# Optimization experiments

Measured on AMD Instinct MI355X. Metric: run time of the kernel, lower is better.

The kernel has to match this reference:

```python
import jax, jax.numpy as jnp
import numpy as np

N_NODES = 50000
N_EDGES = 800000
D_IN = 64
D_OUT = 64


def setup_inputs() -> dict:
    key = jax.random.key(0)
    ks = jax.random.split(key, 7)
    features = jax.random.normal(ks[0], (N_NODES, D_IN), dtype=jnp.float32)
    # Linear(in,out,bias=False) weight: (out_features, in_features)
    W = jax.random.normal(ks[1], (D_OUT, D_IN), dtype=jnp.float32) / np.sqrt(D_IN)
    bias = jnp.zeros((D_OUT,), dtype=jnp.float32)
    skip_weight = jnp.ones((D_OUT,), dtype=jnp.float32)
    # sparse normalized adjacency as an edge list with scalar weights
    edge_src = jax.random.randint(ks[2], (N_EDGES,), 0, N_NODES, dtype=jnp.int32)
    edge_dst = jax.random.randint(ks[3], (N_EDGES,), 0, N_NODES, dtype=jnp.int32)
    edge_weight = jax.random.uniform(ks[4], (N_EDGES,), dtype=jnp.float32)
    return {
        "features": features,
        "W": W,
        "bias": bias,
        "skip_weight": skip_weight,
        "edge_weight": edge_weight,
        "edge_src": edge_src,
        "edge_dst": edge_dst,
    }


def reference(features, W, bias, skip_weight, edge_weight, edge_src, edge_dst):
    # Feature transform: x @ W^T  -> (n, out_features)
    h = jnp.einsum("nd,od->no", features, W)
    # Skip term: elementwise scale of transformed features
    skip = h * skip_weight
    # Sparse SpMM: aggregate weighted neighbor messages
    msgs = h[edge_src] * edge_weight[:, None]          # (E, out)
    agg = jax.ops.segment_sum(msgs, edge_dst, num_segments=N_NODES)  # (n, out)
    out = skip + agg + bias
    return jax.nn.selu(out)
```

## Files before the change

kernel.cpp:

```cpp
#include <hip/hip_runtime.h>
#include <math.h>

#define N_NODES 50000
#define N_EDGES 800000
#define D 64
#define NB2 782
#define BCAP2 2048
#define EPB 4096
#define NSCAT 196
#define CAPB 32
#define SLAB (NSCAT * CAPB)
#define GROWS 128
#define NGEMM ((N_NODES + GROWS - 1) / GROWS)

__device__ __forceinline__ float selu_f(float x) {
    const float scale = 1.0507009873554805f;
    const float alpha = 1.6732632423543772f;
    return x > 0.0f ? scale * x : scale * alpha * expm1f(x);
}

__device__ __forceinline__ unsigned int f2bf(float x) {
    unsigned int u = __float_as_uint(x);
    u += 0x7FFFu + ((u >> 16) & 1u);
    return u >> 16;
}

__device__ __forceinline__ float bf2f(unsigned int b) {
    return __uint_as_float(b << 16);
}

__global__ __launch_bounds__(1024) void fused_gemm_scatter(const float* __restrict__ feat,
                                                           const float* __restrict__ W,
                                                           const int* __restrict__ edst,
                                                           const int* __restrict__ esrc,
                                                           const float* __restrict__ ew,
                                                           unsigned short* __restrict__ hb,
                                                           int* __restrict__ cnts,
                                                           int2* __restrict__ pay) {
    extern __shared__ char smem[];
    const int tid = threadIdx.x;

    if (blockIdx.x < NSCAT) {
        int* hist    = (int*)smem;
        int* lexcl   = hist + NB2;
        int* waveAgg = lexcl + NB2;
        int2* stage  = (int2*)(waveAgg + 16);

        const int wid = tid >> 6;
        const int lane = tid & 63;
        const int e0 = blockIdx.x * EPB;
        const int cntb = min(EPB, N_EDGES - e0);

        for (int i = tid; i < NB2; i += 1024) hist[i] = 0;
        __syncthreads();

        int2 rec[4];
        int rb[4];
#pragma unroll
        for (int k = 0; k < 4; ++k) {
            const int idx = k * 1024 + tid;
            rb[k] = -1;
            if (idx < cntb) {
                const int e = e0 + idx;
                const int dst = edst[e];
                const int b = dst >> 6;
                rb[k] = b;
                rec[k] = make_int2((esrc[e] & 0xFFFF) | ((dst & 63) << 16) | (b << 22),
                                   __float_as_int(ew[e]));
                atomicAdd(&hist[b], 1);
            }
        }
        __syncthreads();

        const int v = (tid < NB2) ? hist[tid] : 0;
        int incl = v;
#pragma unroll
        for (int off = 1; off < 64; off <<= 1) {
            const int t = __shfl_up(incl, off);
            if (lane >= off) incl += t;
        }
        if (lane == 63) waveAgg[wid] = incl;
        __syncthreads();
        if (wid == 0) {
            const int wv = (lane < 16) ? waveAgg[lane] : 0;
            int wincl = wv;
#pragma unroll
            for (int off = 1; off < 16; off <<= 1) {
                const int t = __shfl_up(wincl, off);
                if (lane >= off) wincl += t;
            }
            if (lane < 16) waveAgg[lane] = wincl - wv;
        }
        __syncthreads();
        if (tid < NB2) {
            const int excl = incl - v + waveAgg[wid];
            lexcl[tid] = excl;
            hist[tid] = excl;
            cnts[blockIdx.x * NB2 + tid] = v;
        }
        __syncthreads();

#pragma unroll
        for (int k = 0; k < 4; ++k) {
            if (rb[k] >= 0) {
                const int p = atomicAdd(&hist[rb[k]], 1);
                stage[p] = rec[k];
            }
        }
        __syncthreads();

        for (int i = tid; i < cntb; i += 1024) {
            const int2 r = stage[i];
            const int b = ((unsigned int)r.x) >> 22;
            const int off = i - lexcl[b];
            if (off < CAPB) pay[(size_t)b * SLAB + blockIdx.x * CAPB + off] = r;
        }
    } else {
        float* Wt = (float*)smem;
        float* Sf = Wt + 64 * 68;
        const int base = (blockIdx.x - NSCAT) * GROWS;

        for (int i = tid; i < D * D; i += 1024) {
            int o = i >> 6, d = i & 63;
            Wt[d * 68 + o] = W[i];
        }
        for (int i = tid; i < GROWS * D; i += 1024) {
            int r = i >> 6, c = i & 63;
            int row = base + r;
            Sf[r * 68 + c] = (row < N_NODES) ? feat[(size_t)row * D + c] : 0.0f;
        }
        __syncthreads();

        const int r = tid >> 3;
        const int cg = tid & 7;
        const int row = base + r;
        if (row >= N_NODES) return;

        float4 a0 = {0, 0, 0, 0}, a1 = {0, 0, 0, 0};
        const float* WtC = Wt + cg * 8;
        const float* SfR = Sf + r * 68;
#pragma unroll 8
        for (int k = 0; k < D; ++k) {
            const float f = SfR[k];
            const float4 w0 = *(const float4*)(WtC + k * 68);
            const float4 w1 = *(const float4*)(WtC + k * 68 + 4);
            a0.x += f * w0.x; a0.y += f * w0.y; a0.z += f * w0.z; a0.w += f * w0.w;
            a1.x += f * w1.x; a1.y += f * w1.y; a1.z += f * w1.z; a1.w += f * w1.w;
        }

        uint4 p;
        p.x = f2bf(a0.x) | (f2bf(a0.y) << 16);
        p.y = f2bf(a0.z) | (f2bf(a0.w) << 16);
        p.z = f2bf(a1.x) | (f2bf(a1.y) << 16);
        p.w = f2bf(a1.z) | (f2bf(a1.w) << 16);
        *(uint4*)(hb + (size_t)row * D + cg * 8) = p;
    }
}

__global__ __launch_bounds__(1024) void sort_agg(const int* __restrict__ cnts,
                                                 const int2* __restrict__ pay,
                                                 const unsigned short* __restrict__ hb,
                                                 const float* __restrict__ bias,
                                                 const float* __restrict__ skipw,
                                                 float* __restrict__ out) {
    __shared__ int2 stage[BCAP2];
    __shared__ int2 sorted[BCAP2];
    __shared__ int cntS[NSCAT];
    __shared__ int runoff[NSCAT];
    __shared__ int waveAgg[16];
    __shared__ int cntB[64], begB[64], curB[64];

    const int b = blockIdx.x;
    const int tid = threadIdx.x;
    const int wid = tid >> 6;
    const int lane = tid & 63;
    const int2* payb = pay + (size_t)b * SLAB;

    if (tid < 64) cntB[tid] = 0;

    const int c = (tid < NSCAT) ? cnts[tid * NB2 + b] : 0;

    int incl = c;
#pragma unroll
    for (int off = 1; off < 64; off <<= 1) {
        const int t = __shfl_up(incl, off);
        if (lane >= off) incl += t;
    }
    if (lane == 63) waveAgg[wid] = incl;
    __syncthreads();
    if (wid == 0) {
        const int wv = (lane < 16) ? waveAgg[lane] : 0;
        int wincl = wv;
#pragma unroll
        for (int off = 1; off < 16; off <<= 1) {
            const int t = __shfl_up(wincl, off);
            if (lane >= off) wincl += t;
        }
        if (lane < 16) waveAgg[lane] = wincl - wv;
    }
    __syncthreads();
    if (tid < NSCAT) {
        cntS[tid] = c;
        runoff[tid] = incl - c + waveAgg[wid];
    }
    __syncthreads();

    for (int i = tid; i < NSCAT * CAPB; i += 1024) {
        const int blk = i >> 5;
        const int pos = i & (CAPB - 1);
        if (pos < cntS[blk]) {
            const int p = runoff[blk] + pos;
            if (p < BCAP2) {
                const int2 r = payb[i];
                stage[p] = r;
                atomicAdd(&cntB[(r.x >> 16) & 63], 1);
            }
        }
    }
    __syncthreads();

    const int total = min(runoff[NSCAT - 1] + cntS[NSCAT - 1], BCAP2);

    if (tid < 64) {
        const int v = cntB[tid];
        int inc2 = v;
#pragma unroll
        for (int off = 1; off < 64; off <<= 1) {
            const int t = __shfl_up(inc2, off);
            if (tid >= off) inc2 += t;
        }
        const int excl = inc2 - v;
        begB[tid] = excl;
        curB[tid] = excl;
    }
    __syncthreads();

    for (int i = tid; i < total; i += 1024) {
        const int2 r = stage[i];
        const int p = atomicAdd(&curB[(r.x >> 16) & 63], 1);
        sorted[p] = r;
    }
    __syncthreads();

    const int half = lane >> 5;
    const int sl = lane & 31;
    const float2 kv = ((const float2*)skipw)[sl];
    const float2 bv = ((const float2*)bias)[sl];

    for (int nn = 0; nn < 4; ++nn) {
        const int nl = wid * 4 + nn;
        const int node = (b << 6) + nl;
        if (node >= N_NODES) break;

        const int beg = begB[nl];
        const int deg = cntB[nl];

        float a0x = 0.f, a0y = 0.f, a1x = 0.f, a1y = 0.f;
        float a2x = 0.f, a2y = 0.f, a3x = 0.f, a3y = 0.f;

        int j = 0;
        for (; j + 7 < deg; j += 8) {
            const int2 r0 = sorted[beg + j + 0 + half];
            const int2 r1 = sorted[beg + j + 2 + half];
            const int2 r2 = sorted[beg + j + 4 + half];
            const int2 r3 = sorted[beg + j + 6 + half];
            const unsigned int g0 = *(const unsigned int*)(hb + ((size_t)(r0.x & 0xFFFF) << 6) + sl * 2);
            const unsigned int g1 = *(const unsigned int*)(hb + ((size_t)(r1.x & 0xFFFF) << 6) + sl * 2);
            const unsigned int g2 = *(const unsigned int*)(hb + ((size_t)(r2.x & 0xFFFF) << 6) + sl * 2);
            const unsigned int g3 = *(const unsigned int*)(hb + ((size_t)(r3.x & 0xFFFF) << 6) + sl * 2);
            const float w0 = __int_as_float(r0.y);
            const float w1 = __int_as_float(r1.y);
            const float w2 = __int_as_float(r2.y);
            const float w3 = __int_as_float(r3.y);
            a0x += bf2f(g0 & 0xFFFF) * w0;  a0y += bf2f(g0 >> 16) * w0;
            a1x += bf2f(g1 & 0xFFFF) * w1;  a1y += bf2f(g1 >> 16) * w1;
            a2x += bf2f(g2 & 0xFFFF) * w2;  a2y += bf2f(g2 >> 16) * w2;
            a3x += bf2f(g3 & 0xFFFF) * w3;  a3y += bf2f(g3 >> 16) * w3;
        }
        for (; j + 1 < deg; j += 2) {
            const int2 r = sorted[beg + j + half];
            const unsigned int g = *(const unsigned int*)(hb + ((size_t)(r.x & 0xFFFF) << 6) + sl * 2);
            const float w = __int_as_float(r.y);
            a0x += bf2f(g & 0xFFFF) * w;  a0y += bf2f(g >> 16) * w;
        }
        if (j < deg) {
            const int2 r = sorted[beg + j];
            const unsigned int g = *(const unsigned int*)(hb + ((size_t)(r.x & 0xFFFF) << 6) + sl * 2);
            const float w = __int_as_float(r.y);
            const float m = (half == 0) ? 1.0f : 0.0f;
            a1x += bf2f(g & 0xFFFF) * w * m;  a1y += bf2f(g >> 16) * w * m;
        }

        float sx = (a0x + a1x) + (a2x + a3x);
        float sy = (a0y + a1y) + (a2y + a3y);
        sx += __shfl_xor(sx, 32);
        sy += __shfl_xor(sy, 32);

        if (half == 0) {
            const unsigned int hn = *(const unsigned int*)(hb + ((size_t)node << 6) + sl * 2);
            float2 o;
            o.x = selu_f(bf2f(hn & 0xFFFF) * kv.x + bv.x + sx);
            o.y = selu_f(bf2f(hn >> 16) * kv.y + bv.y + sy);
            ((float2*)(out + ((size_t)node << 6)))[sl] = o;
        }
    }
}

extern "C" void kernel_launch(void* const* d_in, const int* in_sizes, int n_in,
                              void* d_out, int out_size, void* d_ws, size_t ws_size,
                              hipStream_t stream) {
    const float* feat  = (const float*)d_in[0];
    const float* W     = (const float*)d_in[1];
    const float* bias  = (const float*)d_in[2];
    const float* skipw = (const float*)d_in[3];
    const float* ew    = (const float*)d_in[4];
    const int*   esrc  = (const int*)d_in[5];
    const int*   edst  = (const int*)d_in[6];
    float* out = (float*)d_out;

    int2*           pay  = (int2*)d_ws;
    unsigned short* hb   = (unsigned short*)(pay + (size_t)NB2 * SLAB);
    int*            cnts = (int*)(hb + (size_t)N_NODES * D);

    const size_t smem = (size_t)(64 * 68 + GROWS * 68) * sizeof(float);
    fused_gemm_scatter<<<NSCAT + NGEMM, 1024, smem, stream>>>(feat, W, edst, esrc, ew,
                                                              hb, cnts, pay);

    sort_agg<<<NB2, 1024, 0, stream>>>(cnts, pay, hb, bias, skipw, out);
}
```

Before: 125.3 us.

## Replace per-block counting sort with shared-memory float atomic accumulation

```diff
diff --git a/kernel.cpp b/kernel.cpp
--- a/kernel.cpp
+++ b/kernel.cpp
@@ -157,18 +157,17 @@
     }
 }
 
-__global__ __launch_bounds__(1024) void sort_agg(const int* __restrict__ cnts,
-                                                 const int2* __restrict__ pay,
-                                                 const unsigned short* __restrict__ hb,
-                                                 const float* __restrict__ bias,
-                                                 const float* __restrict__ skipw,
-                                                 float* __restrict__ out) {
+__global__ __launch_bounds__(512) void agg_atomic(const int* __restrict__ cnts,
+                                                  const int2* __restrict__ pay,
+                                                  const unsigned short* __restrict__ hb,
+                                                  const float* __restrict__ bias,
+                                                  const float* __restrict__ skipw,
+                                                  float* __restrict__ out) {
     __shared__ int2 stage[BCAP2];
-    __shared__ int2 sorted[BCAP2];
+    __shared__ float acc[64 * 64];
     __shared__ int cntS[NSCAT];
     __shared__ int runoff[NSCAT];
-    __shared__ int waveAgg[16];
-    __shared__ int cntB[64], begB[64], curB[64];
+    __shared__ int waveAgg[8];
 
     const int b = blockIdx.x;
     const int tid = threadIdx.x;
@@ -176,7 +175,7 @@
     const int lane = tid & 63;
     const int2* payb = pay + (size_t)b * SLAB;
 
-    if (tid < 64) cntB[tid] = 0;
+    for (int i = tid; i < 64 * 64; i += 512) acc[i] = 0.0f;
 
     const int c = (tid < NSCAT) ? cnts[tid * NB2 + b] : 0;
 
@@ -189,14 +188,14 @@
     if (lane == 63) waveAgg[wid] = incl;
     __syncthreads();
     if (wid == 0) {
-        const int wv = (lane < 16) ? waveAgg[lane] : 0;
+        const int wv = (lane < 8) ? waveAgg[lane] : 0;
         int wincl = wv;
 #pragma unroll
-        for (int off = 1; off < 16; off <<= 1) {
+        for (int off = 1; off < 8; off <<= 1) {
             const int t = __shfl_up(wincl, off);
             if (lane >= off) wincl += t;
         }
-        if (lane < 16) waveAgg[lane] = wincl - wv;
+        if (lane < 8) waveAgg[lane] = wincl - wv;
     }
     __syncthreads();
     if (tid < NSCAT) {
@@ -205,103 +204,52 @@
     }
     __syncthreads();
 
-    for (int i = tid; i < NSCAT * CAPB; i += 1024) {
+    for (int i = tid; i < NSCAT * CAPB; i += 512) {
         const int blk = i >> 5;
         const int pos = i & (CAPB - 1);
         if (pos < cntS[blk]) {
             const int p = runoff[blk] + pos;
-            if (p < BCAP2) {
-                const int2 r = payb[i];
-                stage[p] = r;
-                atomicAdd(&cntB[(r.x >> 16) & 63], 1);
-            }
+            if (p < BCAP2) stage[p] = payb[i];
         }
     }
     __syncthreads();
 
     const int total = min(runoff[NSCAT - 1] + cntS[NSCAT - 1], BCAP2);
-
-    if (tid < 64) {
-        const int v = cntB[tid];
-        int inc2 = v;
-#pragma unroll
-        for (int off = 1; off < 64; off <<= 1) {
-            const int t = __shfl_up(inc2, off);
-            if (tid >= off) inc2 += t;
-        }
-        const int excl = inc2 - v;
-        begB[tid] = excl;
-        curB[tid] = excl;
-    }
-    __syncthreads();
-
-    for (int i = tid; i < total; i += 1024) {
-        const int2 r = stage[i];
-        const int p = atomicAdd(&curB[(r.x >> 16) & 63], 1);
-        sorted[p] = r;
-    }
-    __syncthreads();
 
     const int half = lane >> 5;
     const int sl = lane & 31;
-    const float2 kv = ((const float2*)skipw)[sl];
-    const float2 bv = ((const float2*)bias)[sl];
-
-    for (int nn = 0; nn < 4; ++nn) {
-        const int nl = wid * 4 + nn;
+    const int ngrp = (total + 3) >> 2;
+    for (int g = wid; g < ngrp; g += 8) {
+        const int i0 = (g << 2) + half;
+        const int i1 = i0 + 2;
+        const int2 r0 = stage[i0 < total ? i0 : 0];
+        const int2 r1 = stage[i1 < total ? i1 : 0];
+        const float w0 = (i0 < total) ? __int_as_float(r0.y) : 0.0f;
+        const float w1 = (i1 < total) ? __int_as_float(r1.y) : 0.0f;
+        const unsigned int g0 = *(const unsigned int*)(hb + ((size_t)(r0.x & 0xFFFF) << 6) + sl * 2);
+        const unsigned int g1 = *(const unsigned int*)(hb + ((size_t)(r1.x & 0xFFFF) << 6) + sl * 2);
+        const int n0 = (r0.x >> 16) & 63;
+        const int n1 = (r1.x >> 16) & 63;
+        atomicAdd(&acc[(n0 << 6) + sl * 2],     bf2f(g0 & 0xFFFF) * w0);
+        atomicAdd(&acc[(n0 << 6) + sl * 2 + 1], bf2f(g0 >> 16)    * w0);
+        atomicAdd(&acc[(n1 << 6) + sl * 2],     bf2f(g1 & 0xFFFF) * w1);
+        atomicAdd(&acc[(n1 << 6) + sl * 2 + 1], bf2f(g1 >> 16)    * w1);
+    }
+    __syncthreads();
+
+    for (int i = tid; i < 64 * 32; i += 512) {
+        const int nl = i >> 5;
+        const int f2 = i & 31;
         const int node = (b << 6) + nl;
-        if (node >= N_NODES) break;
-
-        const int beg = begB[nl];
-        const int deg = cntB[nl];
-
-        float a0x = 0.f, a0y = 0.f, a1x = 0.f, a1y = 0.f;
-        float a2x = 0.f, a2y = 0.f, a3x = 0.f, a3y = 0.f;
-
-        int j = 0;
-        for (; j + 7 < deg; j += 8) {
-            const int2 r0 = sorted[beg + j + 0 + half];
-            const int2 r1 = sorted[beg + j + 2 + half];
-            const int2 r2 = sorted[beg + j + 4 + half];
-            const int2 r3 = sorted[beg + j + 6 + half];
-            const unsigned int g0 = *(const unsigned int*)(hb + ((size_t)(r0.x & 0xFFFF) << 6) + sl * 2);
-            const unsigned int g1 = *(const unsigned int*)(hb + ((size_t)(r1.x & 0xFFFF) << 6) + sl * 2);
-            const unsigned int g2 = *(const unsigned int*)(hb + ((size_t)(r2.x & 0xFFFF) << 6) + sl * 2);
-            const unsigned int g3 = *(const unsigned int*)(hb + ((size_t)(r3.x & 0xFFFF) << 6) + sl * 2);
-            const float w0 = __int_as_float(r0.y);
-            const float w1 = __int_as_float(r1.y);
-            const float w2 = __int_as_float(r2.y);
-            const float w3 = __int_as_float(r3.y);
-            a0x += bf2f(g0 & 0xFFFF) * w0;  a0y += bf2f(g0 >> 16) * w0;
-            a1x += bf2f(g1 & 0xFFFF) * w1;  a1y += bf2f(g1 >> 16) * w1;
-            a2x += bf2f(g2 & 0xFFFF) * w2;  a2y += bf2f(g2 >> 16) * w2;
-            a3x += bf2f(g3 & 0xFFFF) * w3;  a3y += bf2f(g3 >> 16) * w3;
-        }
-        for (; j + 1 < deg; j += 2) {
-            const int2 r = sorted[beg + j + half];
-            const unsigned int g = *(const unsigned int*)(hb + ((size_t)(r.x & 0xFFFF) << 6) + sl * 2);
-            const float w = __int_as_float(r.y);
-            a0x += bf2f(g & 0xFFFF) * w;  a0y += bf2f(g >> 16) * w;
-        }
-        if (j < deg) {
-            const int2 r = sorted[beg + j];
-            const unsigned int g = *(const unsigned int*)(hb + ((size_t)(r.x & 0xFFFF) << 6) + sl * 2);
-            const float w = __int_as_float(r.y);
-            const float m = (half == 0) ? 1.0f : 0.0f;
-            a1x += bf2f(g & 0xFFFF) * w * m;  a1y += bf2f(g >> 16) * w * m;
-        }
-
-        float sx = (a0x + a1x) + (a2x + a3x);
-        float sy = (a0y + a1y) + (a2y + a3y);
-        sx += __shfl_xor(sx, 32);
-        sy += __shfl_xor(sy, 32);
-
-        if (half == 0) {
-            const unsigned int hn = *(const unsigned int*)(hb + ((size_t)node << 6) + sl * 2);
+        if (node < N_NODES) {
+            const unsigned int hn = *(const unsigned int*)(hb + ((size_t)node << 6) + f2 * 2);
+            const float2 kv = ((const float2*)skipw)[f2];
+            const float2 bv = ((const float2*)bias)[f2];
+            const float2 av = *((const float2*)&acc[(nl << 6) + f2 * 2]);
             float2 o;
-            o.x = selu_f(bf2f(hn & 0xFFFF) * kv.x + bv.x + sx);
-            o.y = selu_f(bf2f(hn >> 16) * kv.y + bv.y + sy);
-            ((float2*)(out + ((size_t)node << 6)))[sl] = o;
+            o.x = selu_f(bf2f(hn & 0xFFFF) * kv.x + bv.x + av.x);
+            o.y = selu_f(bf2f(hn >> 16)    * kv.y + bv.y + av.y);
+            ((float2*)(out + ((size_t)node << 6)))[f2] = o;
         }
     }
 }
@@ -326,5 +274,5 @@
     fused_gemm_scatter<<<NSCAT + NGEMM, 1024, smem, stream>>>(feat, W, edst, esrc, ew,
                                                               hb, cnts, pay);
 
-    sort_agg<<<NB2, 1024, 0, stream>>>(cnts, pay, hb, bias, skipw, out);
-}
+    agg_atomic<<<NB2, 512, 0, stream>>>(cnts, pay, hb, bias, skipw, out);
+}
```

Result: slower. 445.9 us (+255.9%).
